# Optimization experiments

Measured on AMD Instinct MI355X. Metric: run time of the kernel, lower is better.

Reference implementation:

```python
import jax, jax.numpy as jnp
import numpy as np

N_N, N_E, N_O, EMB, NLAYERS = 58, 1, 256, 512, 28
N_NODES, N_EDGES, N_GRAPHS = 20000, 640000, 16


def _lin_params(key, fan_in, fan_out):
    k1, k2 = jax.random.split(key)
    bound = 1.0 / np.sqrt(fan_in)
    W = jax.random.uniform(k1, (fan_out, fan_in), jnp.float32, -bound, bound)
    b = jax.random.uniform(k2, (fan_out,), jnp.float32, -bound, bound)
    return W, b


def setup_inputs() -> dict:
    key = jax.random.key(0)
    ks = jax.random.split(key, 12)
    x = jax.random.normal(ks[0], (N_NODES, N_N), jnp.float32)
    edge_index = jax.random.randint(ks[1], (2, N_EDGES), 0, N_NODES, jnp.int64)
    edge_features = jax.random.normal(ks[2], (N_EDGES, N_E), jnp.float32)
    batch_index = jnp.sort(jax.random.randint(ks[3], (N_NODES,), 0, N_GRAPHS, jnp.int64))
    # layer 0: n_n -> n_o
    Wn0, bn0 = _lin_params(ks[4], N_N, N_O)
    We0, be0 = _lin_params(ks[5], N_E, N_O)
    Wm0, bm0 = _lin_params(ks[6], N_O, N_O)
    # layers 1..27 stacked: n_o -> n_o
    L = NLAYERS - 1
    kn = jax.random.split(ks[7], L)
    ke = jax.random.split(ks[8], L)
    km = jax.random.split(ks[9], L)
    Wn, bn = jax.vmap(lambda k: _lin_params(k, N_O, N_O))(kn)
    We, be = jax.vmap(lambda k: _lin_params(k, N_E, N_O))(ke)
    Wm, bm = jax.vmap(lambda k: _lin_params(k, N_O, N_O))(km)
    Wlin, blin = _lin_params(ks[10], N_O, EMB)
    return dict(x=x, edge_index=edge_index, edge_features=edge_features,
                batch_index=batch_index,
                Wn0=Wn0, bn0=bn0, We0=We0, be0=be0, Wm0=Wm0, bm0=bm0,
                Wn=Wn, bn=bn, We=We, be=be, Wm=Wm, bm=bm,
                Wlin=Wlin, blin=blin)


def _graph_conv(h, ef, src, dst, Wn, bn, We, be, Wm, bm):
    # update: lin_nodes(x) + scatter_add(message)
    hn = h @ Wn.T + bn                         # [N, n_o]
    me = ef @ We.T + be                        # [E, n_o]
    m = jnp.tanh((hn[src] * me) @ Wm.T + bm)   # [E, n_o]
    aggr = jax.ops.segment_sum(m, dst, num_segments=h.shape[0])
    return hn + aggr


def reference(x, edge_index, edge_features, batch_index,
              Wn0, bn0, We0, be0, Wm0, bm0,
              Wn, bn, We, be, Wm, bm, Wlin, blin):
    src, dst = edge_index[0], edge_index[1]
    h = _graph_conv(x, edge_features, src, dst, Wn0, bn0, We0, be0, Wm0, bm0)

    def layer(h, p):
        wn, bn_, we, be_, wm, bm_ = p
        return _graph_conv(h, edge_features, src, dst, wn, bn_, we, be_, wm, bm_), None

    h, _ = jax.lax.scan(layer, h, (Wn, bn, We, be, Wm, bm))
    out = h @ Wlin.T + blin                    # [N, EMB]
    # per-graph mean pooling
    sums = jax.ops.segment_sum(out, batch_index, num_segments=N_GRAPHS)
    cnts = jax.ops.segment_sum(jnp.ones((out.shape[0],), out.dtype), batch_index,
                               num_segments=N_GRAPHS)
    return sums / cnts[:, None]
```

## Files before the change

kernel.cpp:

```cpp
#include <hip/hip_runtime.h>
#include <hip/hip_fp16.h>

#define NNODES 20000
#define NEDGES 640000
#define NGRAPHS 16
#define NO     256
#define NNF    58
#define KPAD   64
#define EMBD   512
#define NL     28
#define NB     (NNODES / 4)

typedef __attribute__((ext_vector_type(8))) short bf16x8;
typedef __attribute__((ext_vector_type(4))) float f32x4;

__device__ __forceinline__ unsigned short f2bf(float f) {
    unsigned u = __float_as_uint(f);
    return (unsigned short)((u + 0x7fff + ((u >> 16) & 1)) >> 16);
}
__device__ __forceinline__ float bf2f(unsigned short h) {
    return __uint_as_float(((unsigned)h) << 16);
}

__global__ __launch_bounds__(256) void k_hist(const int* __restrict__ dst, int* __restrict__ counts) {
    int e = blockIdx.x * 256 + threadIdx.x;
    if (e < NEDGES) atomicAdd(&counts[dst[e]], 1);
}

__global__ __launch_bounds__(256) void k_scan(const int* __restrict__ counts, int* __restrict__ offs) {
    __shared__ int part[256];
    int t = threadIdx.x;
    const int CH = (NNODES + 255) / 256;
    int base = t * CH;
    int s = 0;
    for (int i = 0; i < CH; ++i) { int idx = base + i; if (idx < NNODES) s += counts[idx]; }
    part[t] = s;
    __syncthreads();
    if (t == 0) { int acc = 0; for (int i = 0; i < 256; ++i) { int v = part[i]; part[i] = acc; acc += v; } }
    __syncthreads();
    int acc = part[t];
    for (int i = 0; i < CH; ++i) { int idx = base + i; if (idx < NNODES) { offs[idx] = acc; acc += counts[idx]; } }
    if (t == 255) offs[NNODES] = acc;
}

__global__ __launch_bounds__(256) void k_copy(const int* __restrict__ a, int* __restrict__ b, int n) {
    int i = blockIdx.x * 256 + threadIdx.x;
    if (i < n) b[i] = a[i];
}

__global__ __launch_bounds__(256) void k_fill(const int* __restrict__ src, const int* __restrict__ dst,
                                              const float* __restrict__ ef, int* __restrict__ cursor,
                                              int* __restrict__ srcp, float* __restrict__ efp) {
    int e = blockIdx.x * 256 + threadIdx.x;
    if (e < NEDGES) {
        int d = dst[e];
        int pos = atomicAdd(&cursor[d], 1);
        srcp[pos] = src[e];
        efp[pos]  = ef[e];
    }
}

__global__ __launch_bounds__(256) void k_padx(const float* __restrict__ x, float* __restrict__ xpad) {
    int i = blockIdx.x * 256 + threadIdx.x;
    if (i < NNODES * KPAD) {
        int r = i >> 6, c = i & 63;
        xpad[i] = (c < NNF) ? x[r * NNF + c] : 0.f;
    }
}

#define SCL 2.8853900817779268f

__global__ __launch_bounds__(256) void k_prepA(
    const float* __restrict__ Wn0, const float* __restrict__ bn0,
    const float* __restrict__ Wn,  const float* __restrict__ bn,
    unsigned short* __restrict__ Whi, unsigned short* __restrict__ Wlo,
    float* __restrict__ bcat) {
    int gid = blockIdx.x * 256 + threadIdx.x;
    if (gid >= NL * NO * NO) return;
    int l = gid / (NO * NO);
    int rem = gid % (NO * NO);
    int r = rem / NO, k = rem % NO;
    float w;
    if (l == 0) w = (k < NNF) ? Wn0[r * NNF + k] : 0.f;
    else        w = Wn[(size_t)(l - 1) * NO * NO + r * NO + k];
    unsigned short hi = f2bf(w);
    unsigned short lo = f2bf(w - bf2f(hi));
    size_t idx = ((size_t)l * 768 + r) * NO + k;
    Whi[idx] = hi; Wlo[idx] = lo;
    if (k == 0) bcat[l * 768 + r] = (l == 0) ? bn0[r] : bn[(l - 1) * NO + r];
}

__global__ __launch_bounds__(256) void k_prepB(
    const float* __restrict__ Wn0, const float* __restrict__ bn0,
    const float* __restrict__ We0, const float* __restrict__ be0,
    const float* __restrict__ Wm0, const float* __restrict__ bm0,
    const float* __restrict__ Wn,  const float* __restrict__ bn,
    const float* __restrict__ We,  const float* __restrict__ be,
    const float* __restrict__ Wm,  const float* __restrict__ bm,
    unsigned short* __restrict__ Whi, unsigned short* __restrict__ Wlo,
    float* __restrict__ bcat) {
    int l = blockIdx.x >> 5;
    int rr0 = (blockIdx.x & 31) * 16;
    int k = threadIdx.x;
    const float *wn, *bnv, *wev, *bev, *wm, *bmv;
    int K;
    if (l == 0) { wn = Wn0; bnv = bn0; wev = We0; bev = be0; wm = Wm0; bmv = bm0; K = NNF; }
    else {
        int j = l - 1;
        wn = Wn + (size_t)j * NO * NO; bnv = bn + j * NO;
        wev = We + j * NO;             bev = be + j * NO;
        wm = Wm + (size_t)j * NO * NO; bmv = bm + j * NO;
        K = NO;
    }
    __shared__ float coeff[16][NO + 1];
    for (int q = 0; q < 16; ++q) {
        int rr = rr0 + q;
        int i = rr & 255;
        const float* scale = (rr < 256) ? wev : bev;
        coeff[q][k] = wm[(size_t)i * NO + k] * scale[k];
    }
    __syncthreads();
    float acc[16] = {};
    if (k < K) {
        for (int j = 0; j < NO; ++j) {
            float wv = wn[(size_t)j * K + k];
            #pragma unroll
            for (int q = 0; q < 16; ++q) acc[q] += coeff[q][j] * wv;
        }
    }
    for (int q = 0; q < 16; ++q) {
        float w = (k < K) ? acc[q] * SCL : 0.f;
        unsigned short hi = f2bf(w);
        unsigned short lo = f2bf(w - bf2f(hi));
        size_t idx = ((size_t)l * 768 + 256 + rr0 + q) * NO + k;
        Whi[idx] = hi; Wlo[idx] = lo;
    }
    if (k < 16) {
        int rr = rr0 + k;
        int i = rr & 255;
        float b = 0.f;
        for (int j = 0; j < NO; ++j) b += coeff[k][j] * bnv[j];
        if (rr >= 256) b += bmv[i];
        bcat[l * 768 + 256 + rr] = b * SCL;
    }
}

#define LDP 40
__global__ __launch_bounds__(256) void k_gemm(const float* __restrict__ A,
                                              const unsigned short* __restrict__ Whi,
                                              const unsigned short* __restrict__ Wlo,
                                              const float* __restrict__ bias,
                                              float* __restrict__ HN, __half* __restrict__ UV,
                                              int M, int K) {
    __shared__ short sAhi[128 * LDP];
    __shared__ short sAlo[128 * LDP];
    __shared__ short sBhi[128 * LDP];
    __shared__ short sBlo[128 * LDP];
    int bn0 = blockIdx.x * 128;
    int bm0 = blockIdx.y * 128;
    int t = threadIdx.x;
    int wid = t >> 6, lane = t & 63;
    int wr = wid >> 1, wc = wid & 1;
    int lr = lane & 15, lg = lane >> 4;
    int kofs = lg * 8;
    f32x4 acc[4][4] = {};

    int srow = t >> 1, skh = (t & 1) * 16;

    for (int k0 = 0; k0 < K; k0 += 32) {
        {
            int gr = bm0 + srow;
            float f[16];
            if (gr < M) {
                #pragma unroll
                for (int q = 0; q < 4; ++q)
                    *(float4*)(f + 4 * q) = *(const float4*)(A + (size_t)gr * K + k0 + skh + 4 * q);
            } else {
                #pragma unroll
                for (int q = 0; q < 16; ++q) f[q] = 0.f;
            }
            int ph[8], pl[8];
            #pragma unroll
            for (int q = 0; q < 8; ++q) {
                unsigned short h0 = f2bf(f[2 * q]);
                unsigned short h1 = f2bf(f[2 * q + 1]);
                unsigned short l0 = f2bf(f[2 * q] - bf2f(h0));
                unsigned short l1 = f2bf(f[2 * q + 1] - bf2f(h1));
                ph[q] = (int)h0 | ((int)h1 << 16);
                pl[q] = (int)l0 | ((int)l1 << 16);
            }
            *(int4*)(void*)(sAhi + srow * LDP + skh)     = *(int4*)(void*)(ph);
            *(int4*)(void*)(sAhi + srow * LDP + skh + 8) = *(int4*)(void*)(ph + 4);
            *(int4*)(void*)(sAlo + srow * LDP + skh)     = *(int4*)(void*)(pl);
            *(int4*)(void*)(sAlo + srow * LDP + skh + 8) = *(int4*)(void*)(pl + 4);
        }
        {
            const unsigned short* gh = Whi + (size_t)(bn0 + srow) * NO + k0 + skh;
            const unsigned short* gl = Wlo + (size_t)(bn0 + srow) * NO + k0 + skh;
            *(int4*)(void*)(sBhi + srow * LDP + skh)     = *(const int4*)(void*)(gh);
            *(int4*)(void*)(sBhi + srow * LDP + skh + 8) = *(const int4*)(void*)(gh + 8);
            *(int4*)(void*)(sBlo + srow * LDP + skh)     = *(const int4*)(void*)(gl);
            *(int4*)(void*)(sBlo + srow * LDP + skh + 8) = *(const int4*)(void*)(gl + 8);
        }
        __syncthreads();
        bf16x8 ah[4], al[4], wh[4], wl[4];
        #pragma unroll
        for (int f = 0; f < 4; ++f) {
            ah[f] = *(bf16x8*)(void*)(sAhi + (wr * 64 + f * 16 + lr) * LDP + kofs);
            al[f] = *(bf16x8*)(void*)(sAlo + (wr * 64 + f * 16 + lr) * LDP + kofs);
            wh[f] = *(bf16x8*)(void*)(sBhi + (wc * 64 + f * 16 + lr) * LDP + kofs);
            wl[f] = *(bf16x8*)(void*)(sBlo + (wc * 64 + f * 16 + lr) * LDP + kofs);
        }
        #pragma unroll
        for (int fc = 0; fc < 4; ++fc)
            #pragma unroll
            for (int fr = 0; fr < 4; ++fr) {
                acc[fc][fr] = __builtin_amdgcn_mfma_f32_16x16x32_bf16(wh[fc], ah[fr], acc[fc][fr], 0, 0, 0);
                acc[fc][fr] = __builtin_amdgcn_mfma_f32_16x16x32_bf16(wh[fc], al[fr], acc[fc][fr], 0, 0, 0);
                acc[fc][fr] = __builtin_amdgcn_mfma_f32_16x16x32_bf16(wl[fc], ah[fr], acc[fc][fr], 0, 0, 0);
            }
        __syncthreads();
    }
    #pragma unroll
    for (int fc = 0; fc < 4; ++fc) {
        int n0 = bn0 + wc * 64 + fc * 16 + lg * 4;
        float4 bi = *(const float4*)(bias + n0);
        #pragma unroll
        for (int fr = 0; fr < 4; ++fr) {
            int gr = bm0 + wr * 64 + fr * 16 + lr;
            if (gr >= M) continue;
            f32x4 v = acc[fc][fr];
            float o0 = v[0] + bi.x, o1 = v[1] + bi.y, o2 = v[2] + bi.z, o3 = v[3] + bi.w;
            if (n0 < 256) {
                float4 o = {o0, o1, o2, o3};
                *(float4*)(HN + (size_t)gr * NO + n0) = o;
            } else {
                int i0 = (n0 < 512) ? n0 - 256 : n0 - 512;
                int base = 2 * i0 + ((n0 < 512) ? 0 : 4);
                union { __half2 h2[2]; uint2 u; } pk;
                pk.h2[0] = __floats2half2_rn(o0, o1);
                pk.h2[1] = __floats2half2_rn(o2, o3);
                *(uint2*)(UV + (size_t)gr * 512 + base) = pk.u;
            }
        }
    }
}

__global__ __launch_bounds__(256) void k_edge(const float* __restrict__ HN, const __half* __restrict__ UV,
                                              const int* __restrict__ offs,
                                              const int* __restrict__ srcp, const float* __restrict__ efp,
                                              float* __restrict__ hout) {
    int blk = blockIdx.x;
    int pass = blk / NB;
    int nb   = blk - pass * NB;
    int wv = threadIdx.x >> 6;
    int lane = threadIdx.x & 63;
    int n = nb * 4 + wv;
    int es = lane >> 4, cl = lane & 15;
    int e0 = offs[n], e1 = offs[n + 1];
    float a0 = 0.f, a1 = 0.f, a2 = 0.f, a3 = 0.f;
    const __half* uvb = UV + pass * 128 + cl * 8;
    for (int eb = e0; eb < e1; eb += 64) {
        int cnt = e1 - eb; if (cnt > 64) cnt = 64;
        int sv = 0; float fv = 0.f;
        if (lane < cnt) { sv = srcp[eb + lane]; fv = efp[eb + lane]; }
        for (int i = 0; i < cnt; i += 4) {
            int j = i + es;
            int ss = __shfl(sv, j);
            float ff = __shfl(fv, j);
            if (j < cnt) {
                float4 raw = *(const float4*)(uvb + (size_t)ss * 512);
                const __half2* hp = (const __half2*)&raw;
                float2 u01 = __half22float2(hp[0]);
                float2 u23 = __half22float2(hp[1]);
                float2 v01 = __half22float2(hp[2]);
                float2 v23 = __half22float2(hp[3]);
                float g0 = exp2f(fmaf(ff, u01.x, v01.x));
                float g1 = exp2f(fmaf(ff, u01.y, v01.y));
                float g2 = exp2f(fmaf(ff, u23.x, v23.x));
                float g3 = exp2f(fmaf(ff, u23.y, v23.y));
                a0 += 1.0f - 2.0f * __builtin_amdgcn_rcpf(g0 + 1.0f);
                a1 += 1.0f - 2.0f * __builtin_amdgcn_rcpf(g1 + 1.0f);
                a2 += 1.0f - 2.0f * __builtin_amdgcn_rcpf(g2 + 1.0f);
                a3 += 1.0f - 2.0f * __builtin_amdgcn_rcpf(g3 + 1.0f);
            }
        }
    }
    a0 += __shfl_xor(a0, 16); a0 += __shfl_xor(a0, 32);
    a1 += __shfl_xor(a1, 16); a1 += __shfl_xor(a1, 32);
    a2 += __shfl_xor(a2, 16); a2 += __shfl_xor(a2, 32);
    a3 += __shfl_xor(a3, 16); a3 += __shfl_xor(a3, 32);
    if (es == 0) {
        int c0 = pass * 64 + cl * 4;
        float4 hn4 = *(const float4*)(HN + (size_t)n * NO + c0);
        float4 o = {hn4.x + a0, hn4.y + a1, hn4.z + a2, hn4.w + a3};
        *(float4*)(hout + (size_t)n * NO + c0) = o;
    }
}

__device__ __forceinline__ int lower_bound_g(const int* __restrict__ batch, int target) {
    int lo = 0, hi = NNODES;
    while (lo < hi) { int mid = (lo + hi) >> 1; if (batch[mid] < target) lo = mid + 1; else hi = mid; }
    return lo;
}

__global__ __launch_bounds__(256) void k_pool2(const float* __restrict__ h, const int* __restrict__ batch,
                                               float* __restrict__ sums) {
    int g = blockIdx.x, chunk = blockIdx.y;
    __shared__ int sh[2];
    if (threadIdx.x < 2) sh[threadIdx.x] = lower_bound_g(batch, g + (int)threadIdx.x);
    __syncthreads();
    int lo = sh[0], hi = sh[1];
    float acc = 0.f;
    for (int r = lo + chunk; r < hi; r += 8)
        acc += h[(size_t)r * NO + threadIdx.x];
    atomicAdd(&sums[g * NO + threadIdx.x], acc);
}

__global__ __launch_bounds__(512) void k_final(const float* __restrict__ sums, const int* __restrict__ batch,
                                               const float* __restrict__ Wlin, const float* __restrict__ blin,
                                               float* __restrict__ out) {
    int g = blockIdx.x, t = threadIdx.x;
    __shared__ int sh[2];
    __shared__ float m[NO];
    if (t < 2) sh[t] = lower_bound_g(batch, g + t);
    __syncthreads();
    float inv = 1.f / (float)(sh[1] - sh[0]);
    if (t < NO) m[t] = sums[g * NO + t] * inv;
    __syncthreads();
    float acc = blin[t];
    for (int k = 0; k < NO; ++k) acc += m[k] * Wlin[(size_t)t * NO + k];
    out[(size_t)g * EMBD + t] = acc;
}

extern "C" void kernel_launch(void* const* d_in, const int* in_sizes, int n_in,
                              void* d_out, int out_size, void* d_ws, size_t ws_size,
                              hipStream_t stream) {
    const float* x     = (const float*)d_in[0];
    const int*   ei    = (const int*)d_in[1];
    const float* ef    = (const float*)d_in[2];
    const int*   batch = (const int*)d_in[3];
    const float* Wn0 = (const float*)d_in[4];
    const float* bn0 = (const float*)d_in[5];
    const float* We0 = (const float*)d_in[6];
    const float* be0 = (const float*)d_in[7];
    const float* Wm0 = (const float*)d_in[8];
    const float* bm0 = (const float*)d_in[9];
    const float* Wn  = (const float*)d_in[10];
    const float* bn  = (const float*)d_in[11];
    const float* We  = (const float*)d_in[12];
    const float* be  = (const float*)d_in[13];
    const float* Wm  = (const float*)d_in[14];
    const float* bm  = (const float*)d_in[15];
    const float* Wlin = (const float*)d_in[16];
    const float* blin = (const float*)d_in[17];
    float* out = (float*)d_out;

    char* p = (char*)d_ws;
    auto carve = [&](size_t bytes) { char* q = p; p += (bytes + 255) & ~(size_t)255; return q; };
    float*  h    = (float*)carve((size_t)NNODES * NO * 4);
    float*  HN   = (float*)carve((size_t)NNODES * NO * 4);
    __half* UV   = (__half*)carve((size_t)NNODES * 512 * 2);
    unsigned short* Whi = (unsigned short*)carve((size_t)NL * 768 * NO * 2);
    unsigned short* Wlo = (unsigned short*)carve((size_t)NL * 768 * NO * 2);
    float*  bcat = (float*)carve((size_t)NL * 768 * 4);
    float*  xpad = (float*)carve((size_t)NNODES * KPAD * 4);
    int*    offs = (int*)carve((size_t)(NNODES + 1) * 4);
    int*    cur  = (int*)carve((size_t)NNODES * 4);
    int*    srcp = (int*)carve((size_t)NEDGES * 4);
    float*  efp  = (float*)carve((size_t)NEDGES * 4);
    float*  sums = (float*)carve((size_t)NGRAPHS * NO * 4);

    const int* src = ei;
    const int* dst = ei + NEDGES;

    hipMemsetAsync(cur, 0, (size_t)NNODES * 4, stream);
    k_hist<<<NEDGES / 256, 256, 0, stream>>>(dst, cur);
    k_scan<<<1, 256, 0, stream>>>(cur, offs);
    k_copy<<<(NNODES + 255) / 256, 256, 0, stream>>>(offs, cur, NNODES);
    k_fill<<<NEDGES / 256, 256, 0, stream>>>(src, dst, ef, cur, srcp, efp);

    k_padx<<<(NNODES * KPAD + 255) / 256, 256, 0, stream>>>(x, xpad);
    k_prepA<<<(NL * NO * NO + 255) / 256, 256, 0, stream>>>(Wn0, bn0, Wn, bn, Whi, Wlo, bcat);
    k_prepB<<<NL * 32, 256, 0, stream>>>(Wn0, bn0, We0, be0, Wm0, bm0,
                                         Wn, bn, We, be, Wm, bm, Whi, Wlo, bcat);

    for (int l = 0; l < NL; ++l) {
        const float* Ain = (l == 0) ? xpad : h;
        int K = (l == 0) ? KPAD : NO;
        dim3 grid(768 / 128, (NNODES + 127) / 128);
        k_gemm<<<grid, 256, 0, stream>>>(Ain, Whi + (size_t)l * 768 * NO, Wlo + (size_t)l * 768 * NO,
                                         bcat + (size_t)l * 768, HN, UV, NNODES, K);
        k_edge<<<4 * NB, 256, 0, stream>>>(HN, UV, offs, srcp, efp, h);
    }

    hipMemsetAsync(sums, 0, (size_t)NGRAPHS * NO * 4, stream);
    dim3 pg(NGRAPHS, 8);
    k_pool2<<<pg, 256, 0, stream>>>(h, batch, sums);
    k_final<<<NGRAPHS, 512, 0, stream>>>(sums, batch, Wlin, blin, out);
}
```

Before: 3.842 ms.

## Interleave edge metadata and unroll edge loop with half-precision FMA

Packs each edge's source index and feature into one int2 record, so the edge kernel does a single 8-byte load per edge instead of two separate arrays and a shuffle broadcast. The edge loop now has each lane group walk edges directly with stride 4, two edges per iteration, so two gathers are in flight at once. The pre-activation is computed with a packed half2 FMA, and the tanh constant terms are pulled out of the loop (sum of 1 - 2r becomes cnt - 2*sum r), leaving fewer ALU ops per edge. The half-precision FMA and the cast of the edge feature to half lower accuracy.

```diff
diff --git a/kernel.cpp b/kernel.cpp
--- a/kernel.cpp
+++ b/kernel.cpp
@@ -50,13 +50,12 @@
 
 __global__ __launch_bounds__(256) void k_fill(const int* __restrict__ src, const int* __restrict__ dst,
                                               const float* __restrict__ ef, int* __restrict__ cursor,
-                                              int* __restrict__ srcp, float* __restrict__ efp) {
+                                              int2* __restrict__ em) {
     int e = blockIdx.x * 256 + threadIdx.x;
     if (e < NEDGES) {
         int d = dst[e];
         int pos = atomicAdd(&cursor[d], 1);
-        srcp[pos] = src[e];
-        efp[pos]  = ef[e];
+        em[pos] = make_int2(src[e], __float_as_int(ef[e]));
     }
 }
 
@@ -248,7 +247,7 @@
 
 __global__ __launch_bounds__(256) void k_edge(const float* __restrict__ HN, const __half* __restrict__ UV,
                                               const int* __restrict__ offs,
-                                              const int* __restrict__ srcp, const float* __restrict__ efp,
+                                              const int2* __restrict__ em,
                                               float* __restrict__ hout) {
     int blk = blockIdx.x;
     int pass = blk / NB;
@@ -258,42 +257,49 @@
     int n = nb * 4 + wv;
     int es = lane >> 4, cl = lane & 15;
     int e0 = offs[n], e1 = offs[n + 1];
-    float a0 = 0.f, a1 = 0.f, a2 = 0.f, a3 = 0.f;
+    float r0 = 0.f, r1 = 0.f, r2 = 0.f, r3 = 0.f;
     const __half* uvb = UV + pass * 128 + cl * 8;
-    for (int eb = e0; eb < e1; eb += 64) {
-        int cnt = e1 - eb; if (cnt > 64) cnt = 64;
-        int sv = 0; float fv = 0.f;
-        if (lane < cnt) { sv = srcp[eb + lane]; fv = efp[eb + lane]; }
-        for (int i = 0; i < cnt; i += 4) {
-            int j = i + es;
-            int ss = __shfl(sv, j);
-            float ff = __shfl(fv, j);
-            if (j < cnt) {
-                float4 raw = *(const float4*)(uvb + (size_t)ss * 512);
-                const __half2* hp = (const __half2*)&raw;
-                float2 u01 = __half22float2(hp[0]);
-                float2 u23 = __half22float2(hp[1]);
-                float2 v01 = __half22float2(hp[2]);
-                float2 v23 = __half22float2(hp[3]);
-                float g0 = exp2f(fmaf(ff, u01.x, v01.x));
-                float g1 = exp2f(fmaf(ff, u01.y, v01.y));
-                float g2 = exp2f(fmaf(ff, u23.x, v23.x));
-                float g3 = exp2f(fmaf(ff, u23.y, v23.y));
-                a0 += 1.0f - 2.0f * __builtin_amdgcn_rcpf(g0 + 1.0f);
-                a1 += 1.0f - 2.0f * __builtin_amdgcn_rcpf(g1 + 1.0f);
-                a2 += 1.0f - 2.0f * __builtin_amdgcn_rcpf(g2 + 1.0f);
-                a3 += 1.0f - 2.0f * __builtin_amdgcn_rcpf(g3 + 1.0f);
-            }
-        }
-    }
-    a0 += __shfl_xor(a0, 16); a0 += __shfl_xor(a0, 32);
-    a1 += __shfl_xor(a1, 16); a1 += __shfl_xor(a1, 32);
-    a2 += __shfl_xor(a2, 16); a2 += __shfl_xor(a2, 32);
-    a3 += __shfl_xor(a3, 16); a3 += __shfl_xor(a3, 32);
+    for (int e = e0 + es; e < e1; e += 8) {
+        int e2 = e + 4;
+        bool v1 = e2 < e1;
+        int e2c = v1 ? e2 : e;
+        int2 m0 = em[e];
+        int2 m1 = em[e2c];
+        float4 raw0 = *(const float4*)(uvb + (size_t)m0.x * 512);
+        float4 raw1 = *(const float4*)(uvb + (size_t)m1.x * 512);
+        __half2 f0 = __half2half2(__float2half_rn(__int_as_float(m0.y)));
+        const __half2* h0 = (const __half2*)&raw0;
+        __half2 za = __hfma2(f0, h0[0], h0[2]);
+        __half2 zb = __hfma2(f0, h0[1], h0[3]);
+        float2 xa = __half22float2(za);
+        float2 xb = __half22float2(zb);
+        r0 += __builtin_amdgcn_rcpf(exp2f(xa.x) + 1.0f);
+        r1 += __builtin_amdgcn_rcpf(exp2f(xa.y) + 1.0f);
+        r2 += __builtin_amdgcn_rcpf(exp2f(xb.x) + 1.0f);
+        r3 += __builtin_amdgcn_rcpf(exp2f(xb.y) + 1.0f);
+        if (v1) {
+            __half2 f1 = __half2half2(__float2half_rn(__int_as_float(m1.y)));
+            const __half2* h1 = (const __half2*)&raw1;
+            __half2 zc = __hfma2(f1, h1[0], h1[2]);
+            __half2 zd = __hfma2(f1, h1[1], h1[3]);
+            float2 xc = __half22float2(zc);
+            float2 xd = __half22float2(zd);
+            r0 += __builtin_amdgcn_rcpf(exp2f(xc.x) + 1.0f);
+            r1 += __builtin_amdgcn_rcpf(exp2f(xc.y) + 1.0f);
+            r2 += __builtin_amdgcn_rcpf(exp2f(xd.x) + 1.0f);
+            r3 += __builtin_amdgcn_rcpf(exp2f(xd.y) + 1.0f);
+        }
+    }
+    r0 += __shfl_xor(r0, 16); r0 += __shfl_xor(r0, 32);
+    r1 += __shfl_xor(r1, 16); r1 += __shfl_xor(r1, 32);
+    r2 += __shfl_xor(r2, 16); r2 += __shfl_xor(r2, 32);
+    r3 += __shfl_xor(r3, 16); r3 += __shfl_xor(r3, 32);
     if (es == 0) {
+        float cnt = (float)(e1 - e0);
         int c0 = pass * 64 + cl * 4;
         float4 hn4 = *(const float4*)(HN + (size_t)n * NO + c0);
-        float4 o = {hn4.x + a0, hn4.y + a1, hn4.z + a2, hn4.w + a3};
+        float4 o = {hn4.x + cnt - 2.f * r0, hn4.y + cnt - 2.f * r1,
+                    hn4.z + cnt - 2.f * r2, hn4.w + cnt - 2.f * r3};
         *(float4*)(hout + (size_t)n * NO + c0) = o;
     }
 }
@@ -367,8 +373,7 @@
     float*  xpad = (float*)carve((size_t)NNODES * KPAD * 4);
     int*    offs = (int*)carve((size_t)(NNODES + 1) * 4);
     int*    cur  = (int*)carve((size_t)NNODES * 4);
-    int*    srcp = (int*)carve((size_t)NEDGES * 4);
-    float*  efp  = (float*)carve((size_t)NEDGES * 4);
+    int2*   em   = (int2*)carve((size_t)NEDGES * 8);
     float*  sums = (float*)carve((size_t)NGRAPHS * NO * 4);
 
     const int* src = ei;
@@ -378,7 +383,7 @@
     k_hist<<<NEDGES / 256, 256, 0, stream>>>(dst, cur);
     k_scan<<<1, 256, 0, stream>>>(cur, offs);
     k_copy<<<(NNODES + 255) / 256, 256, 0, stream>>>(offs, cur, NNODES);
-    k_fill<<<NEDGES / 256, 256, 0, stream>>>(src, dst, ef, cur, srcp, efp);
+    k_fill<<<NEDGES / 256, 256, 0, stream>>>(src, dst, ef, cur, em);
 
     k_padx<<<(NNODES * KPAD + 255) / 256, 256, 0, stream>>>(x, xpad);
     k_prepA<<<(NL * NO * NO + 255) / 256, 256, 0, stream>>>(Wn0, bn0, Wn, bn, Whi, Wlo, bcat);
@@ -391,7 +396,7 @@
         dim3 grid(768 / 128, (NNODES + 127) / 128);
         k_gemm<<<grid, 256, 0, stream>>>(Ain, Whi + (size_t)l * 768 * NO, Wlo + (size_t)l * 768 * NO,
                                          bcat + (size_t)l * 768, HN, UV, NNODES, K);
-        k_edge<<<4 * NB, 256, 0, stream>>>(HN, UV, offs, srcp, efp, h);
+        k_edge<<<4 * NB, 256, 0, stream>>>(HN, UV, offs, em, h);
     }
 
     hipMemsetAsync(sums, 0, (size_t)NGRAPHS * NO * 4, stream);
```

Measured after the change: 3.976 ms. 1.03x slower.
